# Kernel tuning notes

Measured on AMD Instinct MI355X. Metric: run time of the kernel, lower is better.

Reference implementation:

```python
import jax, jax.numpy as jnp
import numpy as np

EPS = 1e-6  # flax GroupNorm default


def group_norm(x, scale, bias, num_groups):
    B, H, W, C = x.shape
    xg = x.reshape(B, H, W, num_groups, C // num_groups)
    mean = jnp.mean(xg, axis=(1, 2, 4), keepdims=True)
    var = jnp.var(xg, axis=(1, 2, 4), keepdims=True)
    xg = (xg - mean) * jax.lax.rsqrt(var + EPS)
    return xg.reshape(B, H, W, C) * scale + bias


def nin(h, w, b):
    # 1x1 conv / per-pixel dense: bhwc,cd->bhwd
    return jnp.einsum('bhwc,cd->bhwd', h, w) + b


def setup_inputs() -> dict:
    key = jax.random.key(0)
    ks = jax.random.split(key, 8)
    B, H, W, C = 16, 64, 64, 128
    s = 1.0 / np.sqrt(C)
    return {
        'x': jax.random.normal(ks[0], (B, H, W, C), jnp.float32),
        'gn_scale': jnp.ones((C,), jnp.float32),
        'gn_bias': jnp.zeros((C,), jnp.float32),
        'wq': jax.random.normal(ks[1], (C, C), jnp.float32) * s,
        'bq': jnp.zeros((C,), jnp.float32),
        'wk': jax.random.normal(ks[2], (C, C), jnp.float32) * s,
        'bk': jnp.zeros((C,), jnp.float32),
        'wv': jax.random.normal(ks[3], (C, C), jnp.float32) * s,
        'bv': jnp.zeros((C,), jnp.float32),
        'wo': jax.random.normal(ks[4], (C, C), jnp.float32) * s,
        'bo': jnp.zeros((C,), jnp.float32),
    }


def reference(x, gn_scale, gn_bias, wq, bq, wk, bk, wv, bv, wo, bo):
    B, H, W, C = x.shape
    num_groups = min(C // 4, 32)
    h = group_norm(x, gn_scale, gn_bias, num_groups)
    q = nin(h, wq, bq)
    k = nin(h, wk, bk)
    v = nin(h, wv, bv)
    # dense spatial attention; logits (B,H,W,H*W) materialized as in original
    w = jnp.einsum('bhwc,bHWc->bhwHW', q, k) * (C ** -0.5)
    w = w.reshape(B, H, W, H * W)
    w = jax.nn.softmax(w, axis=-1)
    w = w.reshape(B, H, W, H, W)
    h = jnp.einsum('bhwHW,bHWc->bhwc', w, v)
    h = nin(h, wo, bo)
    return x + h  # skip_rescale=False
```

## Files before the change

kernel.cpp:

```cpp
#include <hip/hip_runtime.h>
#include <hip/hip_bf16.h>

typedef unsigned short ushort_t;
typedef unsigned int uint_t;
typedef __attribute__((ext_vector_type(8))) short bf16x8;
typedef __attribute__((ext_vector_type(4))) float f32x4;

#define MFMA32(a, b, c) __builtin_amdgcn_mfma_f32_16x16x32_bf16(a, b, c, 0, 0, 0)

static constexpr int BATCH = 16;
static constexpr int SEQ   = 4096;
static constexpr int CH    = 128;
static constexpr int NGRP  = 32;
static constexpr float EPS = 1e-6f;
static constexpr float C2 = 0.08838834764831845f * 1.4426950408889634f;

__device__ inline ushort_t f2bf(float f) {
    uint_t u = __float_as_uint(f);
    u = (u + 0x7fff + ((u >> 16) & 1)) >> 16;
    return (ushort_t)u;
}

__device__ inline float exp2_fast(float x) {
    return __builtin_amdgcn_exp2f(x);
}

__global__ __launch_bounds__(256) void wprep(const float* __restrict__ W0,
                                             const float* __restrict__ W1,
                                             const float* __restrict__ W2,
                                             const float* __restrict__ W3,
                                             ushort_t* __restrict__ wt) {
    const float* Ws[4] = {W0, W1, W2, W3};
    const float* W = Ws[blockIdx.x];
    ushort_t* out = wt + (size_t)blockIdx.x * CH * CH;
    __shared__ ushort_t tile[128][130];
    int t = threadIdx.x;
    for (int i = 0; i < 16; ++i) {
        int idx = (t + i * 256) * 4;
        int kk = idx >> 7, n = idx & 127;
        float4 w4 = *(const float4*)(W + (size_t)kk * CH + n);
        tile[n + 0][kk] = f2bf(w4.x);
        tile[n + 1][kk] = f2bf(w4.y);
        tile[n + 2][kk] = f2bf(w4.z);
        tile[n + 3][kk] = f2bf(w4.w);
    }
    __syncthreads();
    for (int i = 0; i < 8; ++i) {
        int idx = (t + i * 256) * 8;
        int n = idx >> 7, kk = idx & 127;
        ushort_t tmp[8];
        for (int u = 0; u < 8; ++u) tmp[u] = tile[n][kk + u];
        *(uint4*)&out[(size_t)n * CH + kk] = *(const uint4*)tmp;
    }
}

__global__ void gn_partial(const float* __restrict__ x, float* __restrict__ stats) {
    int bid = blockIdx.x;
    int b = bid >> 4, chunk = bid & 15;
    int t = threadIdx.x;
    int c4 = (t & 31) * 4;
    int rowoff = t >> 5;
    const float* xb = x + (size_t)b * SEQ * CH;
    float s1 = 0.f, s2 = 0.f;
    int base_row = chunk * 256;
    for (int i = 0; i < 32; ++i) {
        int r = base_row + i * 8 + rowoff;
        float4 v = *(const float4*)(xb + (size_t)r * CH + c4);
        s1 += v.x + v.y + v.z + v.w;
        s2 += v.x * v.x + v.y * v.y + v.z * v.z + v.w * v.w;
    }
    __shared__ float red[256][2];
    red[t][0] = s1; red[t][1] = s2;
    __syncthreads();
    if (t < 32) {
        float a1 = 0.f, a2 = 0.f;
        for (int ro = 0; ro < 8; ++ro) {
            a1 += red[ro * 32 + t][0];
            a2 += red[ro * 32 + t][1];
        }
        atomicAdd(&stats[(b * NGRP + t) * 2 + 0], a1);
        atomicAdd(&stats[(b * NGRP + t) * 2 + 1], a2);
    }
}

__global__ __launch_bounds__(256) void gemm_qkv(const float* __restrict__ x,
                                                const float* __restrict__ stats,
                                                const float* __restrict__ gsc,
                                                const float* __restrict__ gbi,
                                                const ushort_t* __restrict__ wt,
                                                const float* __restrict__ Bq,
                                                const float* __restrict__ Bk,
                                                const float* __restrict__ Bv,
                                                ushort_t* __restrict__ outq,
                                                ushort_t* __restrict__ outk,
                                                ushort_t* __restrict__ outvt) {
    __shared__ ushort_t lds_a[128][136];
    __shared__ float2 gstat[32];
    int t = threadIdx.x;
    int wv = t >> 6, lane = t & 63, quad = lane >> 4, l16 = lane & 15;
    size_t m0 = (size_t)blockIdx.x * 128;
    int batch = (int)(m0 >> 12);
    int seq0  = (int)(m0 & 4095);
    if (t < 32) {
        float sum = stats[(batch * NGRP + t) * 2 + 0];
        float sq  = stats[(batch * NGRP + t) * 2 + 1];
        float mean = sum / 16384.f;
        float var  = sq / 16384.f - mean * mean;
        gstat[t] = float2{mean, __frsqrt_rn(var + EPS)};
    }
    __syncthreads();
    for (int i = 0; i < 8; ++i) {
        int idx = (t + i * 256) * 8;
        int r = idx >> 7, c = idx & 127;
        size_t row = m0 + r;
        float4 xa = *(const float4*)(x + row * CH + c);
        float4 xc = *(const float4*)(x + row * CH + c + 4);
        float2 stA = gstat[c >> 2];
        float2 stB = gstat[(c >> 2) + 1];
        float4 sA = *(const float4*)(gsc + c), sB = *(const float4*)(gsc + c + 4);
        float4 bA = *(const float4*)(gbi + c), bB = *(const float4*)(gbi + c + 4);
        ushort_t tmp[8];
        tmp[0] = f2bf((xa.x - stA.x) * stA.y * sA.x + bA.x);
        tmp[1] = f2bf((xa.y - stA.x) * stA.y * sA.y + bA.y);
        tmp[2] = f2bf((xa.z - stA.x) * stA.y * sA.z + bA.z);
        tmp[3] = f2bf((xa.w - stA.x) * stA.y * sA.w + bA.w);
        tmp[4] = f2bf((xc.x - stB.x) * stB.y * sB.x + bB.x);
        tmp[5] = f2bf((xc.y - stB.x) * stB.y * sB.y + bB.y);
        tmp[6] = f2bf((xc.z - stB.x) * stB.y * sB.z + bB.z);
        tmp[7] = f2bf((xc.w - stB.x) * stB.y * sB.w + bB.w);
        *(uint4*)&lds_a[r][c] = *(const uint4*)tmp;
    }
    __syncthreads();
    for (int j = 0; j < 3; ++j) {
        const ushort_t* wtj = wt + (size_t)j * CH * CH;
        const float* Bi = (j == 0) ? Bq : (j == 1) ? Bk : Bv;
        f32x4 acc[2][8] = {};
        for (int kh = 0; kh < 2; ++kh) {
            int k0 = kh * 64;
            for (int ks = 0; ks < 2; ++ks) {
                bf16x8 afrag[2];
                for (int tr = 0; tr < 2; ++tr)
                    afrag[tr] = *(const bf16x8*)&lds_a[wv * 32 + tr * 16 + l16][k0 + ks * 32 + quad * 8];
                for (int tc = 0; tc < 8; ++tc) {
                    bf16x8 bfrag = *(const bf16x8*)(wtj + (size_t)(tc * 16 + l16) * CH + k0 + ks * 32 + quad * 8);
                    for (int tr = 0; tr < 2; ++tr)
                        acc[tr][tc] = MFMA32(afrag[tr], bfrag, acc[tr][tc]);
                }
            }
        }
        for (int tc = 0; tc < 8; ++tc) {
            int col = tc * 16 + l16;
            float bval = Bi[col];
            for (int tr = 0; tr < 2; ++tr) {
                int rl = wv * 32 + tr * 16 + quad * 4;
                if (j == 2) {
                    ushort_t tmp[4];
                    for (int r = 0; r < 4; ++r) tmp[r] = f2bf(acc[tr][tc][r] + bval);
                    *(uint2*)&outvt[(size_t)batch * CH * SEQ + (size_t)col * SEQ + seq0 + rl] =
                        *(const uint2*)tmp;
                } else {
                    ushort_t* op = (j == 0) ? outq : outk;
                    for (int r = 0; r < 4; ++r) {
                        float vv = acc[tr][tc][r] + bval;
                        if (j == 0) vv *= C2;
                        op[(m0 + rl + r) * CH + col] = f2bf(vv);
                    }
                }
            }
        }
    }
}

__global__ __launch_bounds__(256, 2) void flash_attn18(const ushort_t* __restrict__ q,
                                                       const ushort_t* __restrict__ k,
                                                       const ushort_t* __restrict__ vt,
                                                       ushort_t* __restrict__ o) {
    int bid = blockIdx.x;
    int b = bid & 15, qt = bid >> 4;
    int t = threadIdx.x;
    int wv = t >> 6, lane = t & 63, quad = lane >> 4, l16 = lane & 15;
    const size_t SB = (size_t)SEQ * CH;
    const ushort_t* qb  = q  + (size_t)b * SB;
    const ushort_t* kb  = k  + (size_t)b * SB;
    const ushort_t* vtb = vt + (size_t)b * SB;

    __shared__ ushort_t lds_k[2][64][136];
    __shared__ ushort_t lds_vt[2][128][72];

    int qrow_base = qt * 128 + wv * 32;
    bf16x8 qfrag[2][4];
#pragma unroll
    for (int nt = 0; nt < 2; ++nt)
#pragma unroll
        for (int ks = 0; ks < 4; ++ks)
            qfrag[nt][ks] = *(const bf16x8*)(qb + (size_t)(qrow_base + nt * 16 + l16) * CH + ks * 32 + quad * 8);

    f32x4 oacc[8][2] = {};
    float psum[2] = {0.f, 0.f};

    int kr_row  = t >> 4;
    int kr_col  = (t & 15) * 8;
    int vr_d    = t >> 3;
    int vr_beta = t & 7;
    int vc0 = 32 * (vr_beta >> 2) + 16 * (vr_beta & 1) + 4 * ((vr_beta >> 1) & 1);

    const ushort_t* kp = kb + (size_t)kr_row * CH + kr_col;
    const ushort_t* vp = vtb + (size_t)vr_d * SEQ + vr_beta * 8;

    uint4 kr[4], vr[4], k1[4];
#pragma unroll
    for (int i = 0; i < 4; ++i) kr[i] = *(const uint4*)(kp + (size_t)i * 16 * CH);
#pragma unroll
    for (int i = 0; i < 4; ++i) vr[i] = *(const uint4*)(vp + (size_t)i * 32 * SEQ);
#pragma unroll
    for (int i = 0; i < 4; ++i) k1[i] = *(const uint4*)(kp + (size_t)(64 + i * 16) * CH);
    kp += 2 * 64 * CH;
    vp += 64;
#pragma unroll
    for (int i = 0; i < 4; ++i) {
        *(uint4*)&lds_k[0][kr_row + 16 * i][kr_col] = kr[i];
        *(uint4*)&lds_k[1][kr_row + 16 * i][kr_col] = k1[i];
        *(uint2*)&lds_vt[0][vr_d + 32 * i][vc0]     = uint2{vr[i].x, vr[i].y};
        *(uint2*)&lds_vt[0][vr_d + 32 * i][vc0 + 8] = uint2{vr[i].z, vr[i].w};
    }
    __syncthreads();

    bf16x8 pkp[2][2];
    {
        f32x4 s[4][2] = {};
#pragma unroll
        for (int ks = 0; ks < 4; ++ks) {
            bf16x8 kf[4];
#pragma unroll
            for (int kt = 0; kt < 4; ++kt)
                kf[kt] = *(const bf16x8*)&lds_k[0][kt * 16 + l16][ks * 32 + quad * 8];
#pragma unroll
            for (int kt = 0; kt < 4; ++kt) {
                s[kt][0] = MFMA32(kf[kt], qfrag[0][ks], s[kt][0]);
                s[kt][1] = MFMA32(kf[kt], qfrag[1][ks], s[kt][1]);
            }
        }
#pragma unroll
        for (int nt = 0; nt < 2; ++nt) {
            float ps = 0.f;
            uint_t pb[8];
#pragma unroll
            for (int kt = 0; kt < 4; ++kt) {
                float p0 = exp2_fast(s[kt][nt][0]);
                float p1 = exp2_fast(s[kt][nt][1]);
                float p2 = exp2_fast(s[kt][nt][2]);
                float p3 = exp2_fast(s[kt][nt][3]);
                ps += (p0 + p1) + (p2 + p3);
                __hip_bfloat162 h01 = __float22bfloat162_rn(float2{p0, p1});
                __hip_bfloat162 h23 = __float22bfloat162_rn(float2{p2, p3});
                __builtin_memcpy(&pb[kt * 2 + 0], &h01, 4);
                __builtin_memcpy(&pb[kt * 2 + 1], &h23, 4);
            }
            psum[nt] += ps;
            __builtin_memcpy(&pkp[nt][0], &pb[0], 16);
            __builtin_memcpy(&pkp[nt][1], &pb[4], 16);
        }
    }
    __syncthreads();

    for (int it = 0; it < 63; ++it) {
        int knxt = (it + 1) & 1;
        int vcur = it & 1;
#pragma unroll
        for (int i = 0; i < 4; ++i) kr[i] = *(const uint4*)(kp + (size_t)i * 16 * CH);
#pragma unroll
        for (int i = 0; i < 4; ++i) vr[i] = *(const uint4*)(vp + (size_t)i * 32 * SEQ);
        kp += 64 * CH; vp += 64;

        f32x4 s[4][2] = {};
#pragma unroll
        for (int u = 0; u < 4; ++u) {
            bf16x8 kf[4];
#pragma unroll
            for (int kt = 0; kt < 4; ++kt)
                kf[kt] = *(const bf16x8*)&lds_k[knxt][kt * 16 + l16][u * 32 + quad * 8];
#pragma unroll
            for (int kt = 0; kt < 4; ++kt) {
                s[kt][0] = MFMA32(kf[kt], qfrag[0][u], s[kt][0]);
                s[kt][1] = MFMA32(kf[kt], qfrag[1][u], s[kt][1]);
            }
#pragma unroll
            for (int m2 = 0; m2 < 2; ++m2) {
                int mt = u * 2 + m2;
                bf16x8 vf0 = *(const bf16x8*)&lds_vt[vcur][mt * 16 + l16][quad * 8];
                bf16x8 vf1 = *(const bf16x8*)&lds_vt[vcur][mt * 16 + l16][32 + quad * 8];
                oacc[mt][0] = MFMA32(vf0, pkp[0][0], oacc[mt][0]);
                oacc[mt][0] = MFMA32(vf1, pkp[0][1], oacc[mt][0]);
                oacc[mt][1] = MFMA32(vf0, pkp[1][0], oacc[mt][1]);
                oacc[mt][1] = MFMA32(vf1, pkp[1][1], oacc[mt][1]);
            }
        }

#pragma unroll
        for (int nt = 0; nt < 2; ++nt) {
            float ps = 0.f;
            uint_t pb[8];
#pragma unroll
            for (int kt = 0; kt < 4; ++kt) {
                float p0 = exp2_fast(s[kt][nt][0]);
                float p1 = exp2_fast(s[kt][nt][1]);
                float p2 = exp2_fast(s[kt][nt][2]);
                float p3 = exp2_fast(s[kt][nt][3]);
                ps += (p0 + p1) + (p2 + p3);
                __hip_bfloat162 h01 = __float22bfloat162_rn(float2{p0, p1});
                __hip_bfloat162 h23 = __float22bfloat162_rn(float2{p2, p3});
                __builtin_memcpy(&pb[kt * 2 + 0], &h01, 4);
                __builtin_memcpy(&pb[kt * 2 + 1], &h23, 4);
            }
            psum[nt] += ps;
            __builtin_memcpy(&pkp[nt][0], &pb[0], 16);
            __builtin_memcpy(&pkp[nt][1], &pb[4], 16);
        }

#pragma unroll
        for (int i = 0; i < 4; ++i) {
            *(uint4*)&lds_k[vcur][kr_row + 16 * i][kr_col] = kr[i];
            *(uint2*)&lds_vt[knxt][vr_d + 32 * i][vc0]     = uint2{vr[i].x, vr[i].y};
            *(uint2*)&lds_vt[knxt][vr_d + 32 * i][vc0 + 8] = uint2{vr[i].z, vr[i].w};
        }
        __syncthreads();
    }

#pragma unroll
    for (int mt = 0; mt < 8; ++mt) {
        bf16x8 vf0 = *(const bf16x8*)&lds_vt[1][mt * 16 + l16][quad * 8];
        bf16x8 vf1 = *(const bf16x8*)&lds_vt[1][mt * 16 + l16][32 + quad * 8];
        oacc[mt][0] = MFMA32(vf0, pkp[0][0], oacc[mt][0]);
        oacc[mt][0] = MFMA32(vf1, pkp[0][1], oacc[mt][0]);
        oacc[mt][1] = MFMA32(vf0, pkp[1][0], oacc[mt][1]);
        oacc[mt][1] = MFMA32(vf1, pkp[1][1], oacc[mt][1]);
    }

#pragma unroll
    for (int nt = 0; nt < 2; ++nt) {
        float tot = psum[nt];
        tot += __shfl_xor(tot, 16, 64);
        tot += __shfl_xor(tot, 32, 64);
        float inv = 1.f / tot;
        size_t row = (size_t)b * SEQ + qrow_base + nt * 16 + l16;
#pragma unroll
        for (int mt = 0; mt < 8; ++mt) {
            ushort_t tmp[4];
#pragma unroll
            for (int r = 0; r < 4; ++r) tmp[r] = f2bf(oacc[mt][nt][r] * inv);
            *(uint2*)&o[row * CH + mt * 16 + quad * 4] = *(const uint2*)tmp;
        }
    }
}

__global__ __launch_bounds__(256) void gemm_out(const ushort_t* __restrict__ A,
                                                const ushort_t* __restrict__ wto,
                                                const float* __restrict__ bias,
                                                const float* __restrict__ resid,
                                                float* __restrict__ out) {
    __shared__ ushort_t lds_a[128][136];
    int t = threadIdx.x;
    int wv = t >> 6, lane = t & 63, quad = lane >> 4, l16 = lane & 15;
    size_t m0 = (size_t)blockIdx.x * 128;
    for (int i = 0; i < 8; ++i) {
        int idx = (t + i * 256) * 8;
        int r = idx >> 7, c = idx & 127;
        *(uint4*)&lds_a[r][c] = *(const uint4*)(A + (m0 + r) * CH + c);
    }
    __syncthreads();
    f32x4 acc[2][8] = {};
    for (int kh = 0; kh < 2; ++kh) {
        int k0 = kh * 64;
        for (int ks = 0; ks < 2; ++ks) {
            bf16x8 afrag[2];
            for (int tr = 0; tr < 2; ++tr)
                afrag[tr] = *(const bf16x8*)&lds_a[wv * 32 + tr * 16 + l16][k0 + ks * 32 + quad * 8];
            for (int tc = 0; tc < 8; ++tc) {
                bf16x8 bfrag = *(const bf16x8*)(wto + (size_t)(tc * 16 + l16) * CH + k0 + ks * 32 + quad * 8);
                for (int tr = 0; tr < 2; ++tr)
                    acc[tr][tc] = MFMA32(afrag[tr], bfrag, acc[tr][tc]);
            }
        }
    }
    for (int tc = 0; tc < 8; ++tc) {
        int col = tc * 16 + l16;
        float bval = bias[col];
        for (int tr = 0; tr < 2; ++tr) {
            int rl = wv * 32 + tr * 16 + quad * 4;
            for (int r = 0; r < 4; ++r) {
                size_t row = m0 + rl + r;
                out[row * CH + col] = acc[tr][tc][r] + bval + resid[row * CH + col];
            }
        }
    }
}

extern "C" void kernel_launch(void* const* d_in, const int* in_sizes, int n_in,
                              void* d_out, int out_size, void* d_ws, size_t ws_size,
                              hipStream_t stream) {
    const float* x   = (const float*)d_in[0];
    const float* gsc = (const float*)d_in[1];
    const float* gbi = (const float*)d_in[2];
    const float* wq  = (const float*)d_in[3];
    const float* bq  = (const float*)d_in[4];
    const float* wk  = (const float*)d_in[5];
    const float* bk  = (const float*)d_in[6];
    const float* wvp = (const float*)d_in[7];
    const float* bv  = (const float*)d_in[8];
    const float* wo  = (const float*)d_in[9];
    const float* bo  = (const float*)d_in[10];
    float* outp = (float*)d_out;

    const size_t NELEM = (size_t)BATCH * SEQ * CH;
    float*    stats = (float*)d_ws;
    ushort_t* qbuf  = (ushort_t*)((char*)d_ws + 4096);
    ushort_t* kbuf  = qbuf + NELEM;
    ushort_t* vtbuf = kbuf + NELEM;
    ushort_t* abuf  = vtbuf + NELEM;
    ushort_t* wtbuf = abuf + NELEM;

    hipMemsetAsync(stats, 0, BATCH * NGRP * 2 * sizeof(float), stream);
    wprep<<<4, 256, 0, stream>>>(wq, wk, wvp, wo, wtbuf);
    gn_partial<<<256, 256, 0, stream>>>(x, stats);
    gemm_qkv<<<512, 256, 0, stream>>>(x, stats, gsc, gbi, wtbuf, bq, bk, bv,
                                      qbuf, kbuf, vtbuf);
    flash_attn18<<<512, 512 / 2, 0, stream>>>(qbuf, kbuf, vtbuf, abuf);
    gemm_out<<<512, 256, 0, stream>>>(abuf, wtbuf + 3 * CH * CH, bo, x, outp);
}
```

Before: 293.4 us.

## Fuse GN stats with weight prep, drop memset/atomics, use 8-wave GEMM blocks

Merges the weight conversion kernel and the GroupNorm partial-stat kernel into one launch. Per-chunk partial sums are written to dedicated slots and reduced in gemm_qkv, which removes the memset and the atomics. Both projection GEMMs now run 512 threads per block with each wave owning 16 rows instead of 32. This is meant to cut launch overhead and raise occupancy, but each wave now reuses each weight fragment across only one MFMA row tile instead of two.

```diff
diff --git a/kernel.cpp b/kernel.cpp
--- a/kernel.cpp
+++ b/kernel.cpp
@@ -25,39 +25,41 @@
     return __builtin_amdgcn_exp2f(x);
 }
 
-__global__ __launch_bounds__(256) void wprep(const float* __restrict__ W0,
-                                             const float* __restrict__ W1,
-                                             const float* __restrict__ W2,
-                                             const float* __restrict__ W3,
-                                             ushort_t* __restrict__ wt) {
-    const float* Ws[4] = {W0, W1, W2, W3};
-    const float* W = Ws[blockIdx.x];
-    ushort_t* out = wt + (size_t)blockIdx.x * CH * CH;
-    __shared__ ushort_t tile[128][130];
+__global__ __launch_bounds__(256) void gn_wprep(const float* __restrict__ x,
+                                                float* __restrict__ stats,
+                                                const float* __restrict__ W0,
+                                                const float* __restrict__ W1,
+                                                const float* __restrict__ W2,
+                                                const float* __restrict__ W3,
+                                                ushort_t* __restrict__ wt) {
+    int bid = blockIdx.x;
     int t = threadIdx.x;
-    for (int i = 0; i < 16; ++i) {
-        int idx = (t + i * 256) * 4;
-        int kk = idx >> 7, n = idx & 127;
-        float4 w4 = *(const float4*)(W + (size_t)kk * CH + n);
-        tile[n + 0][kk] = f2bf(w4.x);
-        tile[n + 1][kk] = f2bf(w4.y);
-        tile[n + 2][kk] = f2bf(w4.z);
-        tile[n + 3][kk] = f2bf(w4.w);
-    }
-    __syncthreads();
-    for (int i = 0; i < 8; ++i) {
-        int idx = (t + i * 256) * 8;
-        int n = idx >> 7, kk = idx & 127;
-        ushort_t tmp[8];
-        for (int u = 0; u < 8; ++u) tmp[u] = tile[n][kk + u];
-        *(uint4*)&out[(size_t)n * CH + kk] = *(const uint4*)tmp;
-    }
-}
-
-__global__ void gn_partial(const float* __restrict__ x, float* __restrict__ stats) {
-    int bid = blockIdx.x;
+    if (bid >= 256) {
+        int m = bid - 256;
+        const float* Ws[4] = {W0, W1, W2, W3};
+        const float* W = Ws[m];
+        ushort_t* out = wt + (size_t)m * CH * CH;
+        __shared__ ushort_t tile[128][130];
+        for (int i = 0; i < 16; ++i) {
+            int idx = (t + i * 256) * 4;
+            int kk = idx >> 7, n = idx & 127;
+            float4 w4 = *(const float4*)(W + (size_t)kk * CH + n);
+            tile[n + 0][kk] = f2bf(w4.x);
+            tile[n + 1][kk] = f2bf(w4.y);
+            tile[n + 2][kk] = f2bf(w4.z);
+            tile[n + 3][kk] = f2bf(w4.w);
+        }
+        __syncthreads();
+        for (int i = 0; i < 8; ++i) {
+            int idx = (t + i * 256) * 8;
+            int n = idx >> 7, kk = idx & 127;
+            ushort_t tmp[8];
+            for (int u = 0; u < 8; ++u) tmp[u] = tile[n][kk + u];
+            *(uint4*)&out[(size_t)n * CH + kk] = *(const uint4*)tmp;
+        }
+        return;
+    }
     int b = bid >> 4, chunk = bid & 15;
-    int t = threadIdx.x;
     int c4 = (t & 31) * 4;
     int rowoff = t >> 5;
     const float* xb = x + (size_t)b * SEQ * CH;
@@ -78,12 +80,13 @@
             a1 += red[ro * 32 + t][0];
             a2 += red[ro * 32 + t][1];
         }
-        atomicAdd(&stats[(b * NGRP + t) * 2 + 0], a1);
-        atomicAdd(&stats[(b * NGRP + t) * 2 + 1], a2);
-    }
-}
-
-__global__ __launch_bounds__(256) void gemm_qkv(const float* __restrict__ x,
+        float* slot = stats + ((size_t)(b * 16 + chunk) * 32 + t) * 2;
+        slot[0] = a1;
+        slot[1] = a2;
+    }
+}
+
+__global__ __launch_bounds__(512) void gemm_qkv(const float* __restrict__ x,
                                                 const float* __restrict__ stats,
                                                 const float* __restrict__ gsc,
                                                 const float* __restrict__ gbi,
@@ -102,15 +105,19 @@
     int batch = (int)(m0 >> 12);
     int seq0  = (int)(m0 & 4095);
     if (t < 32) {
-        float sum = stats[(batch * NGRP + t) * 2 + 0];
-        float sq  = stats[(batch * NGRP + t) * 2 + 1];
+        float sum = 0.f, sq = 0.f;
+        for (int c = 0; c < 16; ++c) {
+            const float* slot = stats + ((size_t)(batch * 16 + c) * 32 + t) * 2;
+            sum += slot[0];
+            sq  += slot[1];
+        }
         float mean = sum / 16384.f;
         float var  = sq / 16384.f - mean * mean;
         gstat[t] = float2{mean, __frsqrt_rn(var + EPS)};
     }
     __syncthreads();
-    for (int i = 0; i < 8; ++i) {
-        int idx = (t + i * 256) * 8;
+    for (int i = 0; i < 4; ++i) {
+        int idx = (t + i * 512) * 8;
         int r = idx >> 7, c = idx & 127;
         size_t row = m0 + r;
         float4 xa = *(const float4*)(x + row * CH + c);
@@ -134,37 +141,32 @@
     for (int j = 0; j < 3; ++j) {
         const ushort_t* wtj = wt + (size_t)j * CH * CH;
         const float* Bi = (j == 0) ? Bq : (j == 1) ? Bk : Bv;
-        f32x4 acc[2][8] = {};
+        f32x4 acc[8] = {};
         for (int kh = 0; kh < 2; ++kh) {
             int k0 = kh * 64;
             for (int ks = 0; ks < 2; ++ks) {
-                bf16x8 afrag[2];
-                for (int tr = 0; tr < 2; ++tr)
-                    afrag[tr] = *(const bf16x8*)&lds_a[wv * 32 + tr * 16 + l16][k0 + ks * 32 + quad * 8];
+                bf16x8 afrag = *(const bf16x8*)&lds_a[wv * 16 + l16][k0 + ks * 32 + quad * 8];
                 for (int tc = 0; tc < 8; ++tc) {
                     bf16x8 bfrag = *(const bf16x8*)(wtj + (size_t)(tc * 16 + l16) * CH + k0 + ks * 32 + quad * 8);
-                    for (int tr = 0; tr < 2; ++tr)
-                        acc[tr][tc] = MFMA32(afrag[tr], bfrag, acc[tr][tc]);
+                    acc[tc] = MFMA32(afrag, bfrag, acc[tc]);
                 }
             }
         }
+        int rl = wv * 16 + quad * 4;
         for (int tc = 0; tc < 8; ++tc) {
             int col = tc * 16 + l16;
             float bval = Bi[col];
-            for (int tr = 0; tr < 2; ++tr) {
-                int rl = wv * 32 + tr * 16 + quad * 4;
-                if (j == 2) {
-                    ushort_t tmp[4];
-                    for (int r = 0; r < 4; ++r) tmp[r] = f2bf(acc[tr][tc][r] + bval);
-                    *(uint2*)&outvt[(size_t)batch * CH * SEQ + (size_t)col * SEQ + seq0 + rl] =
-                        *(const uint2*)tmp;
-                } else {
-                    ushort_t* op = (j == 0) ? outq : outk;
-                    for (int r = 0; r < 4; ++r) {
-                        float vv = acc[tr][tc][r] + bval;
-                        if (j == 0) vv *= C2;
-                        op[(m0 + rl + r) * CH + col] = f2bf(vv);
-                    }
+            if (j == 2) {
+                ushort_t tmp[4];
+                for (int r = 0; r < 4; ++r) tmp[r] = f2bf(acc[tc][r] + bval);
+                *(uint2*)&outvt[(size_t)batch * CH * SEQ + (size_t)col * SEQ + seq0 + rl] =
+                    *(const uint2*)tmp;
+            } else {
+                ushort_t* op = (j == 0) ? outq : outk;
+                for (int r = 0; r < 4; ++r) {
+                    float vv = acc[tc][r] + bval;
+                    if (j == 0) vv *= C2;
+                    op[(m0 + rl + r) * CH + col] = f2bf(vv);
                 }
             }
         }
@@ -353,7 +355,7 @@
     }
 }
 
-__global__ __launch_bounds__(256) void gemm_out(const ushort_t* __restrict__ A,
+__global__ __launch_bounds__(512) void gemm_out(const ushort_t* __restrict__ A,
                                                 const ushort_t* __restrict__ wto,
                                                 const float* __restrict__ bias,
                                                 const float* __restrict__ resid,
@@ -362,35 +364,30 @@
     int t = threadIdx.x;
     int wv = t >> 6, lane = t & 63, quad = lane >> 4, l16 = lane & 15;
     size_t m0 = (size_t)blockIdx.x * 128;
-    for (int i = 0; i < 8; ++i) {
-        int idx = (t + i * 256) * 8;
+    for (int i = 0; i < 4; ++i) {
+        int idx = (t + i * 512) * 8;
         int r = idx >> 7, c = idx & 127;
         *(uint4*)&lds_a[r][c] = *(const uint4*)(A + (m0 + r) * CH + c);
     }
     __syncthreads();
-    f32x4 acc[2][8] = {};
+    f32x4 acc[8] = {};
     for (int kh = 0; kh < 2; ++kh) {
         int k0 = kh * 64;
         for (int ks = 0; ks < 2; ++ks) {
-            bf16x8 afrag[2];
-            for (int tr = 0; tr < 2; ++tr)
-                afrag[tr] = *(const bf16x8*)&lds_a[wv * 32 + tr * 16 + l16][k0 + ks * 32 + quad * 8];
+            bf16x8 afrag = *(const bf16x8*)&lds_a[wv * 16 + l16][k0 + ks * 32 + quad * 8];
             for (int tc = 0; tc < 8; ++tc) {
                 bf16x8 bfrag = *(const bf16x8*)(wto + (size_t)(tc * 16 + l16) * CH + k0 + ks * 32 + quad * 8);
-                for (int tr = 0; tr < 2; ++tr)
-                    acc[tr][tc] = MFMA32(afrag[tr], bfrag, acc[tr][tc]);
-            }
-        }
-    }
+                acc[tc] = MFMA32(afrag, bfrag, acc[tc]);
+            }
+        }
+    }
+    int rl = wv * 16 + quad * 4;
     for (int tc = 0; tc < 8; ++tc) {
         int col = tc * 16 + l16;
         float bval = bias[col];
-        for (int tr = 0; tr < 2; ++tr) {
-            int rl = wv * 32 + tr * 16 + quad * 4;
-            for (int r = 0; r < 4; ++r) {
-                size_t row = m0 + rl + r;
-                out[row * CH + col] = acc[tr][tc][r] + bval + resid[row * CH + col];
-            }
+        for (int r = 0; r < 4; ++r) {
+            size_t row = m0 + rl + r;
+            out[row * CH + col] = acc[tc][r] + bval + resid[row * CH + col];
         }
     }
 }
@@ -412,18 +409,16 @@
     float* outp = (float*)d_out;
 
     const size_t NELEM = (size_t)BATCH * SEQ * CH;
-    float*    stats = (float*)d_ws;
-    ushort_t* qbuf  = (ushort_t*)((char*)d_ws + 4096);
+    ushort_t* qbuf  = (ushort_t*)d_ws;
     ushort_t* kbuf  = qbuf + NELEM;
     ushort_t* vtbuf = kbuf + NELEM;
     ushort_t* abuf  = vtbuf + NELEM;
     ushort_t* wtbuf = abuf + NELEM;
-
-    hipMemsetAsync(stats, 0, BATCH * NGRP * 2 * sizeof(float), stream);
-    wprep<<<4, 256, 0, stream>>>(wq, wk, wvp, wo, wtbuf);
-    gn_partial<<<256, 256, 0, stream>>>(x, stats);
-    gemm_qkv<<<512, 256, 0, stream>>>(x, stats, gsc, gbi, wtbuf, bq, bk, bv,
+    float*    stats = (float*)(wtbuf + 4 * CH * CH);
+
+    gn_wprep<<<260, 256, 0, stream>>>(x, stats, wq, wk, wvp, wo, wtbuf);
+    gemm_qkv<<<512, 512, 0, stream>>>(x, stats, gsc, gbi, wtbuf, bq, bk, bv,
                                       qbuf, kbuf, vtbuf);
-    flash_attn18<<<512, 512 / 2, 0, stream>>>(qbuf, kbuf, vtbuf, abuf);
-    gemm_out<<<512, 256, 0, stream>>>(abuf, wtbuf + 3 * CH * CH, bo, x, outp);
-}
+    flash_attn18<<<512, 256, 0, stream>>>(qbuf, kbuf, vtbuf, abuf);
+    gemm_out<<<512, 512, 0, stream>>>(abuf, wtbuf + 3 * CH * CH, bo, x, outp);
+}
```

After: 302.8 us. 3.2% more time.
